# Performance work log

Hardware: AMD Instinct MI355X
Metric: run time of the kernel (lower is better)

The kernel has to match this reference:

```python
import jax, jax.numpy as jnp
import numpy as np

D_MODEL = 1024
D_STATE = 256

def setup_inputs() -> dict:
    key = jax.random.key(0)
    k1, k2, k3, k4 = jax.random.split(key, 4)
    x = jax.random.normal(k1, (8, 4096, D_MODEL), dtype=jnp.float32)
    A = jax.random.normal(k2, (D_STATE,), dtype=jnp.float32)
    B = jax.random.normal(k3, (D_STATE, D_MODEL), dtype=jnp.float32) * 0.01
    C = jax.random.normal(k4, (D_MODEL, D_STATE), dtype=jnp.float32) * 0.01
    D = jnp.ones((D_MODEL,), dtype=jnp.float32)
    return {"x": x, "A": A, "B": B, "C": C, "D": D}

def reference(x, A, B, C, D):
    # x: (b, s, d_model)
    a_bar = jnp.exp(-jnp.exp(A))                     # (n,)
    Bx = jnp.einsum('bsd,nd->bsn', x, B)             # (b, s, n) precomputed input drive

    def step(h, bx_t):
        h = a_bar * h + bx_t                          # (b, n)
        return h, h

    h0 = jnp.zeros((x.shape[0], A.shape[0]), dtype=x.dtype)
    # scan over time axis: move seq to leading axis
    _, hs = jax.lax.scan(step, h0, jnp.swapaxes(Bx, 0, 1))  # hs: (s, b, n)
    hs = jnp.swapaxes(hs, 0, 1)                      # (b, s, n)
    y = jnp.einsum('bsn,dn->bsd', hs, C) + D * x     # (b, s, d_model)
    return y
```

## Files before the change

### kernel.cpp

```cpp
#include <hip/hip_runtime.h>
#include <cstdint>
#include <cstddef>


typedef __attribute__((ext_vector_type(8))) _Float16 half8;
typedef __attribute__((ext_vector_type(4))) float f32x4;

__device__ inline half8 cvt8(float4 a, float4 b) {
  half8 h;
  h[0] = (_Float16)a.x; h[1] = (_Float16)a.y;
  h[2] = (_Float16)a.z; h[3] = (_Float16)a.w;
  h[4] = (_Float16)b.x; h[5] = (_Float16)b.y;
  h[6] = (_Float16)b.z; h[7] = (_Float16)b.w;
  return h;
}

__global__ __launch_bounds__(256) void gemm_bx(
    const float* __restrict__ x, const float* __restrict__ Bp,
    _Float16* __restrict__ Bxh)
{
  constexpr int LDT = 40;
  __shared__ __align__(16) _Float16 lA[2][64 * LDT];
  __shared__ __align__(16) _Float16 lB[2][256 * LDT];

  const int tid  = threadIdx.x;
  const int lane = tid & 63;
  const int wave = tid >> 6;
  const int wn   = wave * 64;
  const int quad = lane >> 4;
  const int l16  = lane & 15;
  const long blockM = (long)blockIdx.x * 64;

  const int arow = tid >> 2, akc = (tid & 3) * 8;
  const float* gA = x + (blockM + arow) * 1024 + akc;
  int brow[4], bkc[4];
  const float* gB[4];
  #pragma unroll
  for (int i = 0; i < 4; i++) {
    const int ch = tid + i * 256;
    brow[i] = ch >> 2; bkc[i] = (ch & 3) * 8;
    gB[i] = Bp + brow[i] * 1024 + bkc[i];
  }

  float4 ra0, ra1, rb0[4], rb1[4];
  ra0 = *(const float4*)gA; ra1 = *(const float4*)(gA + 4);
  #pragma unroll
  for (int i = 0; i < 4; i++) {
    rb0[i] = *(const float4*)gB[i]; rb1[i] = *(const float4*)(gB[i] + 4);
  }
  *(half8*)&lA[0][arow * LDT + akc] = cvt8(ra0, ra1);
  #pragma unroll
  for (int i = 0; i < 4; i++)
    *(half8*)&lB[0][brow[i] * LDT + bkc[i]] = cvt8(rb0[i], rb1[i]);
  __syncthreads();

  f32x4 acc[4][4];
  #pragma unroll
  for (int i = 0; i < 4; i++)
    #pragma unroll
    for (int j = 0; j < 4; j++) acc[i][j] = (f32x4){0.f, 0.f, 0.f, 0.f};

  for (int it = 0; it < 32; ++it) {
    const int cur = it & 1;
    if (it < 31) {
      const int k = (it + 1) * 32;
      ra0 = *(const float4*)(gA + k); ra1 = *(const float4*)(gA + k + 4);
      #pragma unroll
      for (int i = 0; i < 4; i++) {
        rb0[i] = *(const float4*)(gB[i] + k);
        rb1[i] = *(const float4*)(gB[i] + k + 4);
      }
    }
    half8 af[4], bf[4];
    #pragma unroll
    for (int mt = 0; mt < 4; mt++)
      af[mt] = *(const half8*)&lA[cur][(mt * 16 + l16) * LDT + quad * 8];
    #pragma unroll
    for (int nt = 0; nt < 4; nt++)
      bf[nt] = *(const half8*)&lB[cur][(wn + nt * 16 + l16) * LDT + quad * 8];
    #pragma unroll
    for (int mt = 0; mt < 4; mt++)
      #pragma unroll
      for (int nt = 0; nt < 4; nt++)
        acc[mt][nt] = __builtin_amdgcn_mfma_f32_16x16x32_f16(
            af[mt], bf[nt], acc[mt][nt], 0, 0, 0);
    if (it < 31) {
      *(half8*)&lA[cur ^ 1][arow * LDT + akc] = cvt8(ra0, ra1);
      #pragma unroll
      for (int i = 0; i < 4; i++)
        *(half8*)&lB[cur ^ 1][brow[i] * LDT + bkc[i]] = cvt8(rb0[i], rb1[i]);
    }
    __syncthreads();
  }

  #pragma unroll
  for (int mt = 0; mt < 4; mt++)
    #pragma unroll
    for (int nt = 0; nt < 4; nt++) {
      const int col = wn + nt * 16 + l16;
      #pragma unroll
      for (int r = 0; r < 4; r++) {
        const long row = blockM + mt * 16 + quad * 4 + r;
        Bxh[row * 256 + col] = (_Float16)acc[mt][nt][r];
      }
    }
}


__global__ __launch_bounds__(256) void scan_E(
    const _Float16* __restrict__ Bxh, const float* __restrict__ Ap,
    float* __restrict__ E)
{
  const int n  = threadIdx.x;
  const int bc = blockIdx.x;
  const float al = expf(-expf(Ap[n]));
  const size_t base = (size_t)bc * 64 * 256 + n;
  float h = 0.f;
  #pragma unroll 8
  for (int t = 0; t < 64; t++)
    h = fmaf(al, h, (float)Bxh[base + (size_t)t * 256]);
  E[(size_t)bc * 256 + n] = h;
}

__global__ __launch_bounds__(256) void scan_prefix(
    const float* __restrict__ E, const float* __restrict__ Ap,
    float* __restrict__ carry)
{
  const int n = threadIdx.x;
  const int b = blockIdx.x;
  const float al = expf(-expf(Ap[n]));
  float aL = al;
  #pragma unroll
  for (int i = 0; i < 6; i++) aL *= aL;
  float run = 0.f;
  for (int c = 0; c < 64; c++) {
    const size_t idx = ((size_t)b * 64 + c) * 256 + n;
    carry[idx] = run;
    run = fmaf(aL, run, E[idx]);
  }
}

__global__ __launch_bounds__(256) void scan_apply(
    _Float16* __restrict__ Bxh, const float* __restrict__ Ap,
    const float* __restrict__ carry)
{
  const int n  = threadIdx.x;
  const int bc = blockIdx.x;
  const float al = expf(-expf(Ap[n]));
  float h = carry[(size_t)bc * 256 + n];
  const size_t base = (size_t)bc * 64 * 256 + n;
  #pragma unroll 8
  for (int t = 0; t < 64; t++) {
    const size_t i = base + (size_t)t * 256;
    h = fmaf(al, h, (float)Bxh[i]);
    Bxh[i] = (_Float16)h;
  }
}

__global__ __launch_bounds__(256) void gemm_y(
    const _Float16* __restrict__ hs, const float* __restrict__ Cp,
    const float* __restrict__ x, const float* __restrict__ Dp,
    float* __restrict__ y)
{
  constexpr int LDT = 40;
  __shared__ __align__(16) _Float16 lA[2][128 * LDT];
  __shared__ __align__(16) _Float16 lB[2][128 * LDT];

  const int tid  = threadIdx.x;
  const int lane = tid & 63;
  const int wave = tid >> 6;
  const int wm   = (wave & 1) * 64;
  const int wn   = (wave >> 1) * 64;
  const int quad = lane >> 4;
  const int l16  = lane & 15;
  const long blockM = (long)blockIdx.x * 128;
  const long blockN = (long)blockIdx.y * 128;

  int ar[2], ak[2];
  const _Float16* gA[2];
  const float* gB[2];
  #pragma unroll
  for (int i = 0; i < 2; i++) {
    const int ch = tid + i * 256;
    ar[i] = ch >> 2; ak[i] = (ch & 3) * 8;
    gA[i] = hs + (blockM + ar[i]) * 256 + ak[i];
    gB[i] = Cp + (blockN + ar[i]) * 256 + ak[i];
  }

  half8 ha[2]; float4 rb0[2], rb1[2];
  #pragma unroll
  for (int i = 0; i < 2; i++) {
    ha[i]  = *(const half8*)gA[i];
    rb0[i] = *(const float4*)gB[i];
    rb1[i] = *(const float4*)(gB[i] + 4);
  }
  #pragma unroll
  for (int i = 0; i < 2; i++) {
    *(half8*)&lA[0][ar[i] * LDT + ak[i]] = ha[i];
    *(half8*)&lB[0][ar[i] * LDT + ak[i]] = cvt8(rb0[i], rb1[i]);
  }
  __syncthreads();

  f32x4 acc[4][4];
  #pragma unroll
  for (int i = 0; i < 4; i++)
    #pragma unroll
    for (int j = 0; j < 4; j++) acc[i][j] = (f32x4){0.f, 0.f, 0.f, 0.f};

  for (int it = 0; it < 8; ++it) {
    const int cur = it & 1;
    if (it < 7) {
      const int k = (it + 1) * 32;
      #pragma unroll
      for (int i = 0; i < 2; i++) {
        ha[i]  = *(const half8*)(gA[i] + k);
        rb0[i] = *(const float4*)(gB[i] + k);
        rb1[i] = *(const float4*)(gB[i] + k + 4);
      }
    }
    half8 af[4], bf[4];
    #pragma unroll
    for (int mt = 0; mt < 4; mt++)
      af[mt] = *(const half8*)&lA[cur][(wm + mt * 16 + l16) * LDT + quad * 8];
    #pragma unroll
    for (int nt = 0; nt < 4; nt++)
      bf[nt] = *(const half8*)&lB[cur][(wn + nt * 16 + l16) * LDT + quad * 8];
    #pragma unroll
    for (int mt = 0; mt < 4; mt++)
      #pragma unroll
      for (int nt = 0; nt < 4; nt++)
        acc[mt][nt] = __builtin_amdgcn_mfma_f32_16x16x32_f16(
            af[mt], bf[nt], acc[mt][nt], 0, 0, 0);
    if (it < 7) {
      #pragma unroll
      for (int i = 0; i < 2; i++) {
        *(half8*)&lA[cur ^ 1][ar[i] * LDT + ak[i]] = ha[i];
        *(half8*)&lB[cur ^ 1][ar[i] * LDT + ak[i]] = cvt8(rb0[i], rb1[i]);
      }
    }
    __syncthreads();
  }

  #pragma unroll
  for (int mt = 0; mt < 4; mt++)
    #pragma unroll
    for (int nt = 0; nt < 4; nt++) {
      const long col = blockN + wn + nt * 16 + l16;
      const float dcol = Dp[col];
      #pragma unroll
      for (int r = 0; r < 4; r++) {
        const long row = blockM + wm + mt * 16 + quad * 4 + r;
        y[row * 1024 + col] = acc[mt][nt][r] + dcol * x[row * 1024 + col];
      }
    }
}

extern "C" void kernel_launch(void* const* d_in, const int* in_sizes, int n_in,
                              void* d_out, int out_size, void* d_ws, size_t ws_size,
                              hipStream_t stream) {
  const float* x  = (const float*)d_in[0];
  const float* Ap = (const float*)d_in[1];
  const float* Bp = (const float*)d_in[2];
  const float* Cp = (const float*)d_in[3];
  const float* Dp = (const float*)d_in[4];
  float* y = (float*)d_out;

  _Float16* Bxh  = (_Float16*)d_ws;
  float*    E    = (float*)((char*)d_ws + (size_t)32768 * 256 * 2);
  float*    carry = E + (size_t)512 * 256;

  gemm_bx   <<<512, 256, 0, stream>>>(x, Bp, Bxh);
  scan_E    <<<512, 256, 0, stream>>>(Bxh, Ap, E);
  scan_prefix<<<8,  256, 0, stream>>>(E, Ap, carry);
  scan_apply<<<512, 256, 0, stream>>>(Bxh, Ap, carry);
  gemm_y<<<dim3(256, 8), 256, 0, stream>>>(Bxh, Cp, x, Dp, y);
}
```

Measured before the change: 367.8 us.

## Pre-convert B/C to fp16 and restructure both GEMMs around LDS-resident weights

```diff
diff --git a/kernel.cpp b/kernel.cpp
--- a/kernel.cpp
+++ b/kernel.cpp
@@ -15,97 +15,86 @@
   return h;
 }
 
+__global__ __launch_bounds__(256) void cvt_bc(
+    const float* __restrict__ Bp, const float* __restrict__ Cp,
+    _Float16* __restrict__ Bh, _Float16* __restrict__ Ch)
+{
+  const int g = blockIdx.x * 256 + threadIdx.x;
+  const size_t off = (size_t)(g & 32767) * 8;
+  const float* src = (g < 32768) ? (Bp + off) : (Cp + off);
+  _Float16*    dst = (g < 32768) ? (Bh + off) : (Ch + off);
+  float4 a = *(const float4*)src;
+  float4 b = *(const float4*)(src + 4);
+  *(half8*)dst = cvt8(a, b);
+}
+
 __global__ __launch_bounds__(256) void gemm_bx(
-    const float* __restrict__ x, const float* __restrict__ Bp,
+    const float* __restrict__ x, const _Float16* __restrict__ Bh,
     _Float16* __restrict__ Bxh)
 {
-  constexpr int LDT = 40;
-  __shared__ __align__(16) _Float16 lA[2][64 * LDT];
-  __shared__ __align__(16) _Float16 lB[2][256 * LDT];
+  __shared__ _Float16 lb[256 * 128];
 
   const int tid  = threadIdx.x;
   const int lane = tid & 63;
   const int wave = tid >> 6;
-  const int wn   = wave * 64;
   const int quad = lane >> 4;
   const int l16  = lane & 15;
   const long blockM = (long)blockIdx.x * 64;
-
-  const int arow = tid >> 2, akc = (tid & 3) * 8;
-  const float* gA = x + (blockM + arow) * 1024 + akc;
-  int brow[4], bkc[4];
-  const float* gB[4];
-  #pragma unroll
-  for (int i = 0; i < 4; i++) {
-    const int ch = tid + i * 256;
-    brow[i] = ch >> 2; bkc[i] = (ch & 3) * 8;
-    gB[i] = Bp + brow[i] * 1024 + bkc[i];
-  }
-
-  float4 ra0, ra1, rb0[4], rb1[4];
-  ra0 = *(const float4*)gA; ra1 = *(const float4*)(gA + 4);
-  #pragma unroll
-  for (int i = 0; i < 4; i++) {
-    rb0[i] = *(const float4*)gB[i]; rb1[i] = *(const float4*)(gB[i] + 4);
-  }
-  *(half8*)&lA[0][arow * LDT + akc] = cvt8(ra0, ra1);
-  #pragma unroll
-  for (int i = 0; i < 4; i++)
-    *(half8*)&lB[0][brow[i] * LDT + bkc[i]] = cvt8(rb0[i], rb1[i]);
+  const long arow = blockM + wave * 16 + l16;
+
+  f32x4 acc[16];
+  #pragma unroll
+  for (int i = 0; i < 16; i++) acc[i] = (f32x4){0.f, 0.f, 0.f, 0.f};
+
+  for (int kc = 0; kc < 8; kc++) {
+    __syncthreads();
+    {
+      const int n = tid;
+      const _Float16* src = Bh + (size_t)n * 1024 + kc * 128;
+      #pragma unroll
+      for (int j = 0; j < 16; j++) {
+        half8 v = *(const half8*)(src + j * 8);
+        const int k8p = j ^ (n & 7);
+        *(half8*)&lb[n * 128 + k8p * 8] = v;
+      }
+    }
+    half8 af[4];
+    #pragma unroll
+    for (int ks = 0; ks < 4; ks++) {
+      const float* ga = x + arow * 1024 + kc * 128 + ks * 32 + quad * 8;
+      float4 a0 = *(const float4*)ga;
+      float4 a1 = *(const float4*)(ga + 4);
+      af[ks] = cvt8(a0, a1);
+    }
+    __syncthreads();
+    #pragma unroll
+    for (int ks = 0; ks < 4; ks++) {
+      #pragma unroll
+      for (int nt = 0; nt < 16; nt++) {
+        const int n   = nt * 16 + l16;
+        const int k8p = (ks * 4 + quad) ^ (n & 7);
+        half8 bf = *(const half8*)&lb[n * 128 + k8p * 8];
+        acc[nt] = __builtin_amdgcn_mfma_f32_16x16x32_f16(af[ks], bf, acc[nt], 0, 0, 0);
+      }
+    }
+  }
+
   __syncthreads();
-
-  f32x4 acc[4][4];
-  #pragma unroll
-  for (int i = 0; i < 4; i++)
-    #pragma unroll
-    for (int j = 0; j < 4; j++) acc[i][j] = (f32x4){0.f, 0.f, 0.f, 0.f};
-
-  for (int it = 0; it < 32; ++it) {
-    const int cur = it & 1;
-    if (it < 31) {
-      const int k = (it + 1) * 32;
-      ra0 = *(const float4*)(gA + k); ra1 = *(const float4*)(gA + k + 4);
-      #pragma unroll
-      for (int i = 0; i < 4; i++) {
-        rb0[i] = *(const float4*)(gB[i] + k);
-        rb1[i] = *(const float4*)(gB[i] + k + 4);
-      }
-    }
-    half8 af[4], bf[4];
-    #pragma unroll
-    for (int mt = 0; mt < 4; mt++)
-      af[mt] = *(const half8*)&lA[cur][(mt * 16 + l16) * LDT + quad * 8];
-    #pragma unroll
-    for (int nt = 0; nt < 4; nt++)
-      bf[nt] = *(const half8*)&lB[cur][(wn + nt * 16 + l16) * LDT + quad * 8];
-    #pragma unroll
-    for (int mt = 0; mt < 4; mt++)
-      #pragma unroll
-      for (int nt = 0; nt < 4; nt++)
-        acc[mt][nt] = __builtin_amdgcn_mfma_f32_16x16x32_f16(
-            af[mt], bf[nt], acc[mt][nt], 0, 0, 0);
-    if (it < 31) {
-      *(half8*)&lA[cur ^ 1][arow * LDT + akc] = cvt8(ra0, ra1);
-      #pragma unroll
-      for (int i = 0; i < 4; i++)
-        *(half8*)&lB[cur ^ 1][brow[i] * LDT + bkc[i]] = cvt8(rb0[i], rb1[i]);
-    }
-    __syncthreads();
-  }
-
-  #pragma unroll
-  for (int mt = 0; mt < 4; mt++)
-    #pragma unroll
-    for (int nt = 0; nt < 4; nt++) {
-      const int col = wn + nt * 16 + l16;
-      #pragma unroll
-      for (int r = 0; r < 4; r++) {
-        const long row = blockM + mt * 16 + quad * 4 + r;
-        Bxh[row * 256 + col] = (_Float16)acc[mt][nt][r];
-      }
-    }
-}
-
+  #pragma unroll
+  for (int nt = 0; nt < 16; nt++)
+    #pragma unroll
+    for (int r = 0; r < 4; r++)
+      lb[(wave * 16 + quad * 4 + r) * 256 + nt * 16 + l16] = (_Float16)acc[nt][r];
+  __syncthreads();
+  {
+    const int row = tid >> 2, seg = tid & 3;
+    _Float16* dst = Bxh + (blockM + row) * 256 + seg * 64;
+    const _Float16* srcl = &lb[row * 256 + seg * 64];
+    #pragma unroll
+    for (int j = 0; j < 8; j++)
+      *(half8*)(dst + j * 8) = *(const half8*)(srcl + j * 8);
+  }
+}
 
 __global__ __launch_bounds__(256) void scan_E(
     const _Float16* __restrict__ Bxh, const float* __restrict__ Ap,
@@ -158,101 +147,78 @@
 }
 
 __global__ __launch_bounds__(256) void gemm_y(
-    const _Float16* __restrict__ hs, const float* __restrict__ Cp,
+    const _Float16* __restrict__ hs, const _Float16* __restrict__ Ch,
     const float* __restrict__ x, const float* __restrict__ Dp,
     float* __restrict__ y)
 {
-  constexpr int LDT = 40;
-  __shared__ __align__(16) _Float16 lA[2][128 * LDT];
-  __shared__ __align__(16) _Float16 lB[2][128 * LDT];
+  __shared__ _Float16 lc[128 * 256];
 
   const int tid  = threadIdx.x;
   const int lane = tid & 63;
   const int wave = tid >> 6;
-  const int wm   = (wave & 1) * 64;
-  const int wn   = (wave >> 1) * 64;
   const int quad = lane >> 4;
   const int l16  = lane & 15;
-  const long blockM = (long)blockIdx.x * 128;
-  const long blockN = (long)blockIdx.y * 128;
-
-  int ar[2], ak[2];
-  const _Float16* gA[2];
-  const float* gB[2];
-  #pragma unroll
-  for (int i = 0; i < 2; i++) {
-    const int ch = tid + i * 256;
-    ar[i] = ch >> 2; ak[i] = (ch & 3) * 8;
-    gA[i] = hs + (blockM + ar[i]) * 256 + ak[i];
-    gB[i] = Cp + (blockN + ar[i]) * 256 + ak[i];
-  }
-
-  half8 ha[2]; float4 rb0[2], rb1[2];
-  #pragma unroll
-  for (int i = 0; i < 2; i++) {
-    ha[i]  = *(const half8*)gA[i];
-    rb0[i] = *(const float4*)gB[i];
-    rb1[i] = *(const float4*)(gB[i] + 4);
-  }
-  #pragma unroll
-  for (int i = 0; i < 2; i++) {
-    *(half8*)&lA[0][ar[i] * LDT + ak[i]] = ha[i];
-    *(half8*)&lB[0][ar[i] * LDT + ak[i]] = cvt8(rb0[i], rb1[i]);
-  }
+  const int slab = blockIdx.x & 7;
+  const int mg   = blockIdx.x >> 3;
+  const int n0   = slab * 128;
+
+  {
+    const int n = tid >> 1, hf = tid & 1;
+    const _Float16* src = Ch + (size_t)(n0 + n) * 256 + hf * 128;
+    #pragma unroll
+    for (int j = 0; j < 16; j++) {
+      half8 v = *(const half8*)(src + j * 8);
+      const int k8p = (hf * 16 + j) ^ (n & 7);
+      *(half8*)&lc[n * 256 + k8p * 8] = v;
+    }
+  }
+
+  float dv[8];
+  #pragma unroll
+  for (int nt = 0; nt < 8; nt++) dv[nt] = Dp[n0 + nt * 16 + l16];
+
   __syncthreads();
 
-  f32x4 acc[4][4];
-  #pragma unroll
-  for (int i = 0; i < 4; i++)
-    #pragma unroll
-    for (int j = 0; j < 4; j++) acc[i][j] = (f32x4){0.f, 0.f, 0.f, 0.f};
-
-  for (int it = 0; it < 8; ++it) {
-    const int cur = it & 1;
-    if (it < 7) {
-      const int k = (it + 1) * 32;
-      #pragma unroll
-      for (int i = 0; i < 2; i++) {
-        ha[i]  = *(const half8*)(gA[i] + k);
-        rb0[i] = *(const float4*)(gB[i] + k);
-        rb1[i] = *(const float4*)(gB[i] + k + 4);
+  for (int i = 0; i < 8; i++) {
+    const long chunk   = (long)mg * 8 + i;
+    const long rowbase = chunk * 64 + wave * 16;
+
+    half8 af[8];
+    #pragma unroll
+    for (int ks = 0; ks < 8; ks++)
+      af[ks] = *(const half8*)(hs + (rowbase + l16) * 256 + ks * 32 + quad * 8);
+
+    float xv[4][8];
+    #pragma unroll
+    for (int r = 0; r < 4; r++) {
+      const float* gx = x + (rowbase + quad * 4 + r) * 1024 + n0 + l16;
+      #pragma unroll
+      for (int nt = 0; nt < 8; nt++) xv[r][nt] = gx[nt * 16];
+    }
+
+    f32x4 acc[8];
+    #pragma unroll
+    for (int nt = 0; nt < 8; nt++) acc[nt] = (f32x4){0.f, 0.f, 0.f, 0.f};
+
+    #pragma unroll
+    for (int ks = 0; ks < 8; ks++) {
+      #pragma unroll
+      for (int nt = 0; nt < 8; nt++) {
+        const int n   = nt * 16 + l16;
+        const int k8p = (ks * 4 + quad) ^ (n & 7);
+        half8 bf = *(const half8*)&lc[n * 256 + k8p * 8];
+        acc[nt] = __builtin_amdgcn_mfma_f32_16x16x32_f16(af[ks], bf, acc[nt], 0, 0, 0);
       }
     }
-    half8 af[4], bf[4];
-    #pragma unroll
-    for (int mt = 0; mt < 4; mt++)
-      af[mt] = *(const half8*)&lA[cur][(wm + mt * 16 + l16) * LDT + quad * 8];
-    #pragma unroll
-    for (int nt = 0; nt < 4; nt++)
-      bf[nt] = *(const half8*)&lB[cur][(wn + nt * 16 + l16) * LDT + quad * 8];
-    #pragma unroll
-    for (int mt = 0; mt < 4; mt++)
-      #pragma unroll
-      for (int nt = 0; nt < 4; nt++)
-        acc[mt][nt] = __builtin_amdgcn_mfma_f32_16x16x32_f16(
-            af[mt], bf[nt], acc[mt][nt], 0, 0, 0);
-    if (it < 7) {
-      #pragma unroll
-      for (int i = 0; i < 2; i++) {
-        *(half8*)&lA[cur ^ 1][ar[i] * LDT + ak[i]] = ha[i];
-        *(half8*)&lB[cur ^ 1][ar[i] * LDT + ak[i]] = cvt8(rb0[i], rb1[i]);
-      }
-    }
-    __syncthreads();
-  }
-
-  #pragma unroll
-  for (int mt = 0; mt < 4; mt++)
-    #pragma unroll
-    for (int nt = 0; nt < 4; nt++) {
-      const long col = blockN + wn + nt * 16 + l16;
-      const float dcol = Dp[col];
-      #pragma unroll
-      for (int r = 0; r < 4; r++) {
-        const long row = blockM + wm + mt * 16 + quad * 4 + r;
-        y[row * 1024 + col] = acc[mt][nt][r] + dcol * x[row * 1024 + col];
-      }
-    }
+
+    #pragma unroll
+    for (int r = 0; r < 4; r++) {
+      float* gy = y + (rowbase + quad * 4 + r) * 1024 + n0 + l16;
+      #pragma unroll
+      for (int nt = 0; nt < 8; nt++)
+        gy[nt * 16] = acc[nt][r] + dv[nt] * xv[r][nt];
+    }
+  }
 }
 
 extern "C" void kernel_launch(void* const* d_in, const int* in_sizes, int n_in,
@@ -265,13 +231,16 @@
   const float* Dp = (const float*)d_in[4];
   float* y = (float*)d_out;
 
-  _Float16* Bxh  = (_Float16*)d_ws;
-  float*    E    = (float*)((char*)d_ws + (size_t)32768 * 256 * 2);
-  float*    carry = E + (size_t)512 * 256;
-
-  gemm_bx   <<<512, 256, 0, stream>>>(x, Bp, Bxh);
-  scan_E    <<<512, 256, 0, stream>>>(Bxh, Ap, E);
-  scan_prefix<<<8,  256, 0, stream>>>(E, Ap, carry);
-  scan_apply<<<512, 256, 0, stream>>>(Bxh, Ap, carry);
-  gemm_y<<<dim3(256, 8), 256, 0, stream>>>(Bxh, Cp, x, Dp, y);
-}
+  _Float16* Bxh = (_Float16*)d_ws;
+  _Float16* Bh  = Bxh + (size_t)32768 * 256;
+  _Float16* Ch  = Bh + (size_t)256 * 1024;
+  float* E      = (float*)(Ch + (size_t)1024 * 256);
+  float* carry  = E + (size_t)512 * 256;
+
+  cvt_bc     <<<256, 256, 0, stream>>>(Bp, Cp, Bh, Ch);
+  gemm_bx    <<<512, 256, 0, stream>>>(x, Bh, Bxh);
+  scan_E     <<<512, 256, 0, stream>>>(Bxh, Ap, E);
+  scan_prefix<<<8,   256, 0, stream>>>(E, Ap, carry);
+  scan_apply <<<512, 256, 0, stream>>>(Bxh, Ap, carry);
+  gemm_y     <<<512, 256, 0, stream>>>(Bxh, Ch, x, Dp, y);
+}
```

Result: faster. 348.6 us (-5.2%).
